# Optimization experiments

Hardware: AMD Instinct MI355X
Metric: run time of the kernel (lower is better)

## Reference

```python
import jax, jax.numpy as jnp
import numpy as np

# Adaptive embedding (Transformer-XL / wt103 config)
N_TOKEN = 267735
D_PROJ = 1024
CUTOFF_ENDS = [0, 20000, 40000, 200000, N_TOKEN]
DIV_VAL = 4
D_EMBS = [1024 // DIV_VAL**i for i in range(4)]  # [1024, 256, 64, 16]
EMB_SCALE = float(D_PROJ) ** 0.5


def setup_inputs() -> dict:
    key = jax.random.key(0)
    ks = jax.random.split(key, 9)
    inp = jax.random.randint(ks[0], (4, 4096), 0, N_TOKEN, dtype=jnp.int64)
    out = {"inp": inp}
    # init_scale=1.0 -> embed std = d_emb_i**-0.5, proj std = d_proj**-0.5
    for i in range(4):
        l, r = CUTOFF_ENDS[i], CUTOFF_ENDS[i + 1]
        d_i = D_EMBS[i]
        out[f"emb{i}"] = (jax.random.normal(ks[1 + i], (r - l, d_i), dtype=jnp.float32)
                           * (d_i ** -0.5))
        out[f"proj{i}"] = (jax.random.normal(ks[5 + i], (D_PROJ, d_i), dtype=jnp.float32)
                            * (D_PROJ ** -0.5))
    return out


def reference(inp, emb0, emb1, emb2, emb3, proj0, proj1, proj2, proj3):
    embs = [emb0, emb1, emb2, emb3]
    projs = [proj0, proj1, proj2, proj3]
    B, S = inp.shape
    out = jnp.zeros((B, S, D_PROJ), dtype=emb0.dtype)
    for i in range(4):
        l, r = CUTOFF_ENDS[i], CUTOFF_ENDS[i + 1]
        mask = (inp >= l) & (inp < r)                      # [B,S]
        idx = jnp.clip(inp - l, 0, r - l - 1)              # in-range local ids
        e = embs[i][idx]                                   # [B,S,d_i]
        p = jnp.einsum('bsd,pd->bsp', e, projs[i])         # [B,S,d_proj]
        out = out + jnp.where(mask[..., None], p, jnp.zeros((), dtype=p.dtype))
    return out * jnp.asarray(EMB_SCALE, dtype=out.dtype)
```

## Files before the change

### kernel.cpp

```cpp
#include <hip/hip_runtime.h>
#include <stdint.h>

#define NTOKENS 16384
#define DPROJ   1024

#define CAP0 2048
#define CAP1 2048
#define CAP2 12288
#define CAP3 6144
#define TOTCAP 22528

typedef __attribute__((ext_vector_type(8))) short bf16x8;
typedef __attribute__((ext_vector_type(4))) float f32x4;

__device__ __forceinline__ unsigned short f2bf(float f) {
    union { float f; uint32_t u; } x; x.f = f;
    uint32_t r = x.u + 0x7FFFu + ((x.u >> 16) & 1u);
    return (unsigned short)(r >> 16);
}

__device__ __forceinline__ int cap_base(int c) {
    return c == 0 ? 0 : c == 1 ? CAP0 : c == 2 ? CAP0 + CAP1 : CAP0 + CAP1 + CAP2;
}
__device__ __forceinline__ int d_orig(int c) { return 1024 >> (2 * c); }
__device__ __forceinline__ int d_pad(int c)  { return c >= 2 ? 64 : (1024 >> (2 * c)); }


__global__ __launch_bounds__(64) void zero_counts(int* counts) {
    if (threadIdx.x < 4) counts[threadIdx.x] = 0;
}

__global__ __launch_bounds__(256) void scatter_tokens(const int* __restrict__ inp,
                                                      int* counts, uint32_t* tokmap) {
    __shared__ int lcnt[4];
    __shared__ int lbase[4];
    const int t = blockIdx.x * 256 + threadIdx.x;
    if (threadIdx.x < 4) lcnt[threadIdx.x] = 0;
    __syncthreads();
    const int v = inp[t];
    int c, lo;
    if (v < 20000)       { c = 0; lo = 0; }
    else if (v < 40000)  { c = 1; lo = 20000; }
    else if (v < 200000) { c = 2; lo = 40000; }
    else                 { c = 3; lo = 200000; }
    const int lr = atomicAdd(&lcnt[c], 1);
    __syncthreads();
    if (threadIdx.x < 4) lbase[threadIdx.x] = atomicAdd(&counts[threadIdx.x], lcnt[threadIdx.x]);
    __syncthreads();
    const int slot = lbase[c] + lr;
    const int cap = (c == 0 || c == 1) ? CAP0 : (c == 2 ? CAP2 : CAP3);
    if (slot < cap)
        tokmap[cap_base(c) + slot] = ((uint32_t)(v - lo) << 14) | (uint32_t)t;
}

__global__ __launch_bounds__(256) void mfma_gemm(
    const float* __restrict__ e0, const float* __restrict__ e1,
    const float* __restrict__ e2, const float* __restrict__ e3,
    const float* __restrict__ p0, const float* __restrict__ p1,
    const float* __restrict__ p2, const float* __restrict__ p3,
    const int* __restrict__ counts, const uint32_t* __restrict__ tokmap,
    float* __restrict__ out)
{
    const int slot = blockIdx.x;
    const int c  = slot < 32 ? 0 : slot < 64 ? 1 : slot < 256 ? 2 : 3;
    const int tm = slot - (c == 0 ? 0 : c == 1 ? 32 : c == 2 ? 64 : 256);
    const int n  = counts[c];
    if (tm * 64 >= n) return;
    const int tn = blockIdx.y;
    const int d  = d_orig(c);
    const int dp = d_pad(c);
    const float* __restrict__ emb  = c == 0 ? e0 : c == 1 ? e1 : c == 2 ? e2 : e3;
    const float* __restrict__ proj = c == 0 ? p0 : c == 1 ? p1 : c == 2 ? p2 : p3;
    const int cb = cap_base(c);

    __shared__ unsigned short Als[64 * 64];
    __shared__ unsigned short Bls[64 * 64];
    __shared__ int aLoc[64];
    __shared__ int aTok[64];

    const int t = threadIdx.x;
    const int w = t >> 6;
    const int l = t & 63;
    const int wr = w >> 1, wc = w & 1;
    const int g   = l >> 4;
    const int sub = l & 15;

    if (t < 64) {
        const int gr = tm * 64 + t;
        if (gr < n) {
            const uint32_t info = tokmap[cb + gr];
            aLoc[t] = (int)(info >> 14);
            aTok[t] = (int)(info & 16383u);
        } else { aLoc[t] = -1; aTok[t] = -1; }
    }
    __syncthreads();

    f32x4 acc[2][2];
    #pragma unroll
    for (int i = 0; i < 2; ++i)
        #pragma unroll
        for (int j = 0; j < 2; ++j) acc[i][j] = (f32x4)0.f;

    for (int k0 = 0; k0 < dp; k0 += 64) {
        const int kk = k0 + sub * 4;
        #pragma unroll
        for (int pass = 0; pass < 4; ++pass) {
            const int row = w * 16 + pass * 4 + g;
            const int loc = aLoc[row];
            float4 v = make_float4(0.f, 0.f, 0.f, 0.f);
            if (loc >= 0 && kk < d)
                v = *reinterpret_cast<const float4*>(emb + (size_t)loc * d + kk);
            ushort4 o; o.x = f2bf(v.x); o.y = f2bf(v.y); o.z = f2bf(v.z); o.w = f2bf(v.w);
            *reinterpret_cast<ushort4*>((char*)Als + row * 128 +
                ((((sub >> 1) ^ (row & 7)) << 4) | ((sub & 1) << 3))) = o;
        }
        #pragma unroll
        for (int pass = 0; pass < 4; ++pass) {
            const int row = w * 16 + pass * 4 + g;
            float4 v = make_float4(0.f, 0.f, 0.f, 0.f);
            if (kk < d)
                v = *reinterpret_cast<const float4*>(proj + (size_t)(tn * 64 + row) * d + kk);
            ushort4 o; o.x = f2bf(v.x); o.y = f2bf(v.y); o.z = f2bf(v.z); o.w = f2bf(v.w);
            *reinterpret_cast<ushort4*>((char*)Bls + row * 128 +
                ((((sub >> 1) ^ (row & 7)) << 4) | ((sub & 1) << 3))) = o;
        }
        __syncthreads();

        bf16x8 af[2][2], bf[2][2];
        #pragma unroll
        for (int fm = 0; fm < 2; ++fm) {
            const int row = wr * 32 + fm * 16 + (l & 15);
            #pragma unroll
            for (int h = 0; h < 2; ++h) {
                const int chunk = h * 4 + (l >> 4);
                af[fm][h] = *reinterpret_cast<const bf16x8*>(
                    (const char*)Als + row * 128 + ((chunk ^ (row & 7)) << 4));
            }
        }
        #pragma unroll
        for (int fn = 0; fn < 2; ++fn) {
            const int row = wc * 32 + fn * 16 + (l & 15);
            #pragma unroll
            for (int h = 0; h < 2; ++h) {
                const int chunk = h * 4 + (l >> 4);
                bf[fn][h] = *reinterpret_cast<const bf16x8*>(
                    (const char*)Bls + row * 128 + ((chunk ^ (row & 7)) << 4));
            }
        }
        #pragma unroll
        for (int fm = 0; fm < 2; ++fm)
            #pragma unroll
            for (int fn = 0; fn < 2; ++fn)
                #pragma unroll
                for (int h = 0; h < 2; ++h)
                    acc[fm][fn] = __builtin_amdgcn_mfma_f32_16x16x32_bf16(
                        af[fm][h], bf[fn][h], acc[fm][fn], 0, 0, 0);
        __syncthreads();
    }

    const float scale = 32.0f;
    #pragma unroll
    for (int fm = 0; fm < 2; ++fm) {
        const int rbase = wr * 32 + fm * 16 + (l >> 4) * 4;
        #pragma unroll
        for (int r = 0; r < 4; ++r) {
            const int row = rbase + r;
            const int tok = aTok[row];
            if (tok >= 0) {
                float* __restrict__ orow =
                    out + (size_t)tok * DPROJ + tn * 64 + wc * 32 + (l & 15);
                #pragma unroll
                for (int fn = 0; fn < 2; ++fn)
                    orow[fn * 16] = acc[fm][fn][r] * scale;
            }
        }
    }
}

extern "C" void kernel_launch(void* const* d_in, const int* in_sizes, int n_in,
                              void* d_out, int out_size, void* d_ws, size_t ws_size,
                              hipStream_t stream) {
    const int* inp = (const int*)d_in[0];
    const float* emb[4];
    const float* proj[4];
    if (in_sizes[2] == 1024 * 1024) {
        for (int i = 0; i < 4; ++i) { emb[i] = (const float*)d_in[1 + 2 * i];
                                      proj[i] = (const float*)d_in[2 + 2 * i]; }
    } else {
        for (int i = 0; i < 4; ++i) { emb[i] = (const float*)d_in[1 + i];
                                      proj[i] = (const float*)d_in[5 + i]; }
    }
    float* out = (float*)d_out;

    int*      counts = (int*)d_ws;
    uint32_t* tokmap = (uint32_t*)((char*)d_ws + 256);

    zero_counts<<<1, 64, 0, stream>>>(counts);
    scatter_tokens<<<NTOKENS / 256, 256, 0, stream>>>(inp, counts, tokmap);
    mfma_gemm<<<dim3(352, 16), 256, 0, stream>>>(
        emb[0], emb[1], emb[2], emb[3],
        proj[0], proj[1], proj[2], proj[3],
        counts, tokmap, out);
}
```

Baseline: 242.6 us.

## Pre-convert projections to bf16, double-buffer LDS, and widen N tile to 128

Adds a kernel that converts all projection matrices to padded bf16 in workspace once per call. The GEMM then stages B tiles directly into LDS with global_load_lds and double-buffers both A and B across K steps, so the next tile's loads overlap with the MFMAs on the current one. The N tile doubles to 128, which halves the number of gathers of the embedding rows. The cost is one extra launch, extra workspace traffic and more LDS and registers per block.

```diff
diff --git a/kernel.cpp b/kernel.cpp
--- a/kernel.cpp
+++ b/kernel.cpp
@@ -19,12 +19,23 @@
     return (unsigned short)(r >> 16);
 }
 
+__device__ __forceinline__ void gl_lds16(const void* g, void* lds) {
+    __builtin_amdgcn_global_load_lds(
+        (const __attribute__((address_space(1))) void*)g,
+        (__attribute__((address_space(3))) void*)lds, 16, 0, 0);
+}
+
 __device__ __forceinline__ int cap_base(int c) {
     return c == 0 ? 0 : c == 1 ? CAP0 : c == 2 ? CAP0 + CAP1 : CAP0 + CAP1 + CAP2;
 }
 __device__ __forceinline__ int d_orig(int c) { return 1024 >> (2 * c); }
 __device__ __forceinline__ int d_pad(int c)  { return c >= 2 ? 64 : (1024 >> (2 * c)); }
-
+__device__ __forceinline__ size_t p_base(int c) {
+    return c == 0 ? 0u : c == 1 ? 1048576u : c == 2 ? 1310720u : 1376256u;
+}
+
+#define WS_TOKMAP 256
+#define WS_PROJ   92160
 
 __global__ __launch_bounds__(64) void zero_counts(int* counts) {
     if (threadIdx.x < 4) counts[threadIdx.x] = 0;
@@ -53,11 +64,29 @@
         tokmap[cap_base(c) + slot] = ((uint32_t)(v - lo) << 14) | (uint32_t)t;
 }
 
+__global__ __launch_bounds__(256) void conv_proj(const float* __restrict__ p0, const float* __restrict__ p1,
+                                                 const float* __restrict__ p2, const float* __restrict__ p3,
+                                                 unsigned short* __restrict__ projws) {
+    const int c = blockIdx.y;
+    const float* __restrict__ src = c == 0 ? p0 : c == 1 ? p1 : c == 2 ? p2 : p3;
+    const int d  = d_orig(c);
+    const int dp = d_pad(c);
+    const int sh = c == 0 ? 10 : c == 1 ? 8 : 6;
+    const int idx4 = (blockIdx.x * 256 + threadIdx.x) * 4;
+    if (idx4 >= 1024 * dp) return;
+    const int row = idx4 >> sh;
+    const int k   = idx4 & (dp - 1);
+    float4 v = make_float4(0.f, 0.f, 0.f, 0.f);
+    if (k < d) v = *reinterpret_cast<const float4*>(src + (size_t)row * d + k);
+    ushort4 o;
+    o.x = f2bf(v.x); o.y = f2bf(v.y); o.z = f2bf(v.z); o.w = f2bf(v.w);
+    *reinterpret_cast<ushort4*>(projws + p_base(c) + idx4) = o;
+}
+
 __global__ __launch_bounds__(256) void mfma_gemm(
     const float* __restrict__ e0, const float* __restrict__ e1,
     const float* __restrict__ e2, const float* __restrict__ e3,
-    const float* __restrict__ p0, const float* __restrict__ p1,
-    const float* __restrict__ p2, const float* __restrict__ p3,
+    const unsigned short* __restrict__ projws,
     const int* __restrict__ counts, const uint32_t* __restrict__ tokmap,
     float* __restrict__ out)
 {
@@ -69,12 +98,13 @@
     const int tn = blockIdx.y;
     const int d  = d_orig(c);
     const int dp = d_pad(c);
-    const float* __restrict__ emb  = c == 0 ? e0 : c == 1 ? e1 : c == 2 ? e2 : e3;
-    const float* __restrict__ proj = c == 0 ? p0 : c == 1 ? p1 : c == 2 ? p2 : p3;
+    const int nsteps = dp >> 6;
+    const float* __restrict__ emb = c == 0 ? e0 : c == 1 ? e1 : c == 2 ? e2 : e3;
+    const unsigned short* __restrict__ Bsrc = projws + p_base(c) + (size_t)(tn * 128) * dp;
     const int cb = cap_base(c);
 
-    __shared__ unsigned short Als[64 * 64];
-    __shared__ unsigned short Bls[64 * 64];
+    __shared__ unsigned short Als[2][64 * 64];
+    __shared__ unsigned short Bls[2][128 * 64];
     __shared__ int aLoc[64];
     __shared__ int aTok[64];
 
@@ -82,8 +112,6 @@
     const int w = t >> 6;
     const int l = t & 63;
     const int wr = w >> 1, wc = w & 1;
-    const int g   = l >> 4;
-    const int sub = l & 15;
 
     if (t < 64) {
         const int gr = tm * 64 + t;
@@ -95,67 +123,102 @@
     }
     __syncthreads();
 
-    f32x4 acc[2][2];
+    const int arow = t >> 2;
+    const int asl0 = t & 3;
+
+    const int bR0   = l >> 3;
+    const int bphys = l & 7;
+    #define STAGE_B(buf, k0)                                                        \
+        do {                                                                        \
+            _Pragma("unroll")                                                       \
+            for (int i_ = 0; i_ < 4; ++i_) {                                        \
+                const int seg_ = w * 4 + i_;                                        \
+                const int R_   = seg_ * 8 + bR0;                                    \
+                const int src_ = bphys ^ (R_ & 7);                                  \
+                gl_lds16(Bsrc + (size_t)R_ * dp + (k0) + src_ * 8,                  \
+                         &Bls[buf][seg_ * 512]);                                    \
+            }                                                                       \
+        } while (0)
+
+    #define LOAD_A(k0, va)                                                          \
+        do {                                                                        \
+            const int loc_ = aLoc[arow];                                            \
+            _Pragma("unroll")                                                       \
+            for (int i_ = 0; i_ < 4; ++i_) {                                        \
+                const int s_  = asl0 + 4 * i_;                                      \
+                const int kk_ = (k0) + s_ * 4;                                      \
+                va[i_] = make_float4(0.f, 0.f, 0.f, 0.f);                           \
+                if (loc_ >= 0 && kk_ < d)                                           \
+                    va[i_] = *reinterpret_cast<const float4*>(                      \
+                        emb + (size_t)loc_ * d + kk_);                              \
+            }                                                                       \
+        } while (0)
+
+    #define WRITE_A(buf, va)                                                        \
+        do {                                                                        \
+            _Pragma("unroll")                                                       \
+            for (int i_ = 0; i_ < 4; ++i_) {                                        \
+                const int s_ = asl0 + 4 * i_;                                       \
+                const int ch_ = (s_ >> 1) ^ (arow & 7);                             \
+                ushort4 o_;                                                         \
+                o_.x = f2bf(va[i_].x); o_.y = f2bf(va[i_].y);                       \
+                o_.z = f2bf(va[i_].z); o_.w = f2bf(va[i_].w);                       \
+                *reinterpret_cast<ushort4*>((char*)&Als[buf][0] + arow * 128 +      \
+                    ch_ * 16 + (s_ & 1) * 8) = o_;                                  \
+            }                                                                       \
+        } while (0)
+
+    f32x4 acc[2][4];
     #pragma unroll
     for (int i = 0; i < 2; ++i)
         #pragma unroll
-        for (int j = 0; j < 2; ++j) acc[i][j] = (f32x4)0.f;
-
-    for (int k0 = 0; k0 < dp; k0 += 64) {
-        const int kk = k0 + sub * 4;
-        #pragma unroll
-        for (int pass = 0; pass < 4; ++pass) {
-            const int row = w * 16 + pass * 4 + g;
-            const int loc = aLoc[row];
-            float4 v = make_float4(0.f, 0.f, 0.f, 0.f);
-            if (loc >= 0 && kk < d)
-                v = *reinterpret_cast<const float4*>(emb + (size_t)loc * d + kk);
-            ushort4 o; o.x = f2bf(v.x); o.y = f2bf(v.y); o.z = f2bf(v.z); o.w = f2bf(v.w);
-            *reinterpret_cast<ushort4*>((char*)Als + row * 128 +
-                ((((sub >> 1) ^ (row & 7)) << 4) | ((sub & 1) << 3))) = o;
-        }
-        #pragma unroll
-        for (int pass = 0; pass < 4; ++pass) {
-            const int row = w * 16 + pass * 4 + g;
-            float4 v = make_float4(0.f, 0.f, 0.f, 0.f);
-            if (kk < d)
-                v = *reinterpret_cast<const float4*>(proj + (size_t)(tn * 64 + row) * d + kk);
-            ushort4 o; o.x = f2bf(v.x); o.y = f2bf(v.y); o.z = f2bf(v.z); o.w = f2bf(v.w);
-            *reinterpret_cast<ushort4*>((char*)Bls + row * 128 +
-                ((((sub >> 1) ^ (row & 7)) << 4) | ((sub & 1) << 3))) = o;
-        }
-        __syncthreads();
-
-        bf16x8 af[2][2], bf[2][2];
+        for (int j = 0; j < 4; ++j) acc[i][j] = (f32x4)0.f;
+
+    float4 va[4];
+    STAGE_B(0, 0);
+    LOAD_A(0, va);
+    WRITE_A(0, va);
+    __syncthreads();
+
+    int cur = 0;
+    for (int k = 0; k < nsteps; ++k) {
+        const int k0n = (k + 1) << 6;
+        if (k + 1 < nsteps) {
+            STAGE_B(cur ^ 1, k0n);
+            LOAD_A(k0n, va);
+        }
+        bf16x8 af[2][2], bf[4][2];
         #pragma unroll
         for (int fm = 0; fm < 2; ++fm) {
             const int row = wr * 32 + fm * 16 + (l & 15);
             #pragma unroll
             for (int h = 0; h < 2; ++h) {
-                const int chunk = h * 4 + (l >> 4);
+                const int chunk = (h * 4 + (l >> 4)) ^ (row & 7);
                 af[fm][h] = *reinterpret_cast<const bf16x8*>(
-                    (const char*)Als + row * 128 + ((chunk ^ (row & 7)) << 4));
+                    (const char*)&Als[cur][0] + row * 128 + chunk * 16);
             }
         }
         #pragma unroll
-        for (int fn = 0; fn < 2; ++fn) {
-            const int row = wc * 32 + fn * 16 + (l & 15);
+        for (int fn = 0; fn < 4; ++fn) {
+            const int row = wc * 64 + fn * 16 + (l & 15);
             #pragma unroll
             for (int h = 0; h < 2; ++h) {
-                const int chunk = h * 4 + (l >> 4);
+                const int chunk = (h * 4 + (l >> 4)) ^ (row & 7);
                 bf[fn][h] = *reinterpret_cast<const bf16x8*>(
-                    (const char*)Bls + row * 128 + ((chunk ^ (row & 7)) << 4));
+                    (const char*)&Bls[cur][0] + row * 128 + chunk * 16);
             }
         }
         #pragma unroll
         for (int fm = 0; fm < 2; ++fm)
             #pragma unroll
-            for (int fn = 0; fn < 2; ++fn)
+            for (int fn = 0; fn < 4; ++fn)
                 #pragma unroll
                 for (int h = 0; h < 2; ++h)
                     acc[fm][fn] = __builtin_amdgcn_mfma_f32_16x16x32_bf16(
                         af[fm][h], bf[fn][h], acc[fm][fn], 0, 0, 0);
+        if (k + 1 < nsteps) WRITE_A(cur ^ 1, va);
         __syncthreads();
+        cur ^= 1;
     }
 
     const float scale = 32.0f;
@@ -164,13 +227,12 @@
         const int rbase = wr * 32 + fm * 16 + (l >> 4) * 4;
         #pragma unroll
         for (int r = 0; r < 4; ++r) {
-            const int row = rbase + r;
-            const int tok = aTok[row];
+            const int tok = aTok[rbase + r];
             if (tok >= 0) {
                 float* __restrict__ orow =
-                    out + (size_t)tok * DPROJ + tn * 64 + wc * 32 + (l & 15);
+                    out + (size_t)tok * DPROJ + tn * 128 + wc * 64 + (l & 15);
                 #pragma unroll
-                for (int fn = 0; fn < 2; ++fn)
+                for (int fn = 0; fn < 4; ++fn)
                     orow[fn * 16] = acc[fm][fn][r] * scale;
             }
         }
@@ -192,13 +254,14 @@
     }
     float* out = (float*)d_out;
 
-    int*      counts = (int*)d_ws;
-    uint32_t* tokmap = (uint32_t*)((char*)d_ws + 256);
+    int*            counts = (int*)d_ws;
+    uint32_t*       tokmap = (uint32_t*)((char*)d_ws + WS_TOKMAP);
+    unsigned short* projws = (unsigned short*)((char*)d_ws + WS_PROJ);
 
     zero_counts<<<1, 64, 0, stream>>>(counts);
     scatter_tokens<<<NTOKENS / 256, 256, 0, stream>>>(inp, counts, tokmap);
-    mfma_gemm<<<dim3(352, 16), 256, 0, stream>>>(
+    conv_proj<<<dim3(1024, 4), 256, 0, stream>>>(proj[0], proj[1], proj[2], proj[3], projws);
+    mfma_gemm<<<dim3(352, 8), 256, 0, stream>>>(
         emb[0], emb[1], emb[2], emb[3],
-        proj[0], proj[1], proj[2], proj[3],
-        counts, tokmap, out);
-}
+        projws, counts, tokmap, out);
+}
```

Measured after the change: 208.2 us. -14.2%, faster.

## Pre-convert projections to bf16 and load MFMA operands directly from global

Applied to the files above, without the earlier changes.

Adds a pre-pass that converts all projection matrices to bf16 in workspace, folded into the counts-zeroing launch. The GEMM now drops LDS staging and barriers: each lane loads its A fragment straight from the gathered embedding rows, converting to bf16 in registers, and loads B fragments directly from the bf16 projection buffer. The N tile is doubled to 128, so the grid has half as many columns, and the kernel gets a launch-bounds occupancy hint. The aim is to cut repeated fp32 projection reads and conversions plus LDS sync overhead. The cost is uncoalesced per-lane global loads with no reuse through shared memory, and an extra conversion pass over about 1.4M elements on every call.

```diff
diff --git a/kernel.cpp b/kernel.cpp
--- a/kernel.cpp
+++ b/kernel.cpp
@@ -22,12 +22,31 @@
 __device__ __forceinline__ int cap_base(int c) {
     return c == 0 ? 0 : c == 1 ? CAP0 : c == 2 ? CAP0 + CAP1 : CAP0 + CAP1 + CAP2;
 }
-__device__ __forceinline__ int d_orig(int c) { return 1024 >> (2 * c); }
-__device__ __forceinline__ int d_pad(int c)  { return c >= 2 ? 64 : (1024 >> (2 * c)); }
+#define PB1 1048576
+#define PB2 1310720
+#define PB3 1376256
+#define PEND 1392640
+__device__ __forceinline__ size_t p_base(int c) {
+    return c == 0 ? 0u : c == 1 ? (size_t)PB1 : c == 2 ? (size_t)PB2 : (size_t)PB3;
+}
 
+#define WS_TOKMAP 256
+#define WS_PROJ   92160
 
-__global__ __launch_bounds__(64) void zero_counts(int* counts) {
-    if (threadIdx.x < 4) counts[threadIdx.x] = 0;
+__global__ __launch_bounds__(256) void conv_zero(
+    const float* __restrict__ p0, const float* __restrict__ p1,
+    const float* __restrict__ p2, const float* __restrict__ p3,
+    int* counts, unsigned short* __restrict__ projws)
+{
+    if (blockIdx.x == 0 && threadIdx.x < 4) counts[threadIdx.x] = 0;
+    const int idx4 = (blockIdx.x * 256 + threadIdx.x) * 4;
+    const int c = idx4 < PB1 ? 0 : idx4 < PB2 ? 1 : idx4 < PB3 ? 2 : 3;
+    const float* __restrict__ src = c == 0 ? p0 : c == 1 ? p1 : c == 2 ? p2 : p3;
+    const int local = idx4 - (int)p_base(c);
+    float4 v = *reinterpret_cast<const float4*>(src + local);
+    ushort4 o;
+    o.x = f2bf(v.x); o.y = f2bf(v.y); o.z = f2bf(v.z); o.w = f2bf(v.w);
+    *reinterpret_cast<ushort4*>(projws + idx4) = o;
 }
 
 __global__ __launch_bounds__(256) void scatter_tokens(const int* __restrict__ inp,
@@ -53,11 +72,10 @@
         tokmap[cap_base(c) + slot] = ((uint32_t)(v - lo) << 14) | (uint32_t)t;
 }
 
-__global__ __launch_bounds__(256) void mfma_gemm(
+__global__ __launch_bounds__(256, 4) void mfma_gemm(
     const float* __restrict__ e0, const float* __restrict__ e1,
     const float* __restrict__ e2, const float* __restrict__ e3,
-    const float* __restrict__ p0, const float* __restrict__ p1,
-    const float* __restrict__ p2, const float* __restrict__ p3,
+    const unsigned short* __restrict__ projws,
     const int* __restrict__ counts, const uint32_t* __restrict__ tokmap,
     float* __restrict__ out)
 {
@@ -67,110 +85,86 @@
     const int n  = counts[c];
     if (tm * 64 >= n) return;
     const int tn = blockIdx.y;
-    const int d  = d_orig(c);
-    const int dp = d_pad(c);
-    const float* __restrict__ emb  = c == 0 ? e0 : c == 1 ? e1 : c == 2 ? e2 : e3;
-    const float* __restrict__ proj = c == 0 ? p0 : c == 1 ? p1 : c == 2 ? p2 : p3;
+    const int d  = 1024 >> (2 * c);
+    const float* __restrict__ emb = c == 0 ? e0 : c == 1 ? e1 : c == 2 ? e2 : e3;
+    const unsigned short* __restrict__ Bsrc = projws + p_base(c) + (size_t)(tn * 128) * d;
     const int cb = cap_base(c);
-
-    __shared__ unsigned short Als[64 * 64];
-    __shared__ unsigned short Bls[64 * 64];
-    __shared__ int aLoc[64];
-    __shared__ int aTok[64];
 
     const int t = threadIdx.x;
     const int w = t >> 6;
     const int l = t & 63;
     const int wr = w >> 1, wc = w & 1;
-    const int g   = l >> 4;
-    const int sub = l & 15;
+    const int lr = l & 15;
+    const int lg = l >> 4;
 
-    if (t < 64) {
-        const int gr = tm * 64 + t;
-        if (gr < n) {
-            const uint32_t info = tokmap[cb + gr];
-            aLoc[t] = (int)(info >> 14);
-            aTok[t] = (int)(info & 16383u);
-        } else { aLoc[t] = -1; aTok[t] = -1; }
+    const float* arow0;
+    const float* arow1;
+    {
+        const int g0 = tm * 64 + wr * 32 + lr;
+        const int g1 = g0 + 16;
+        arow0 = (g0 < n) ? emb + (size_t)(tokmap[cb + g0] >> 14) * d : nullptr;
+        arow1 = (g1 < n) ? emb + (size_t)(tokmap[cb + g1] >> 14) * d : nullptr;
     }
-    __syncthreads();
 
-    f32x4 acc[2][2];
+    f32x4 acc[2][4];
     #pragma unroll
     for (int i = 0; i < 2; ++i)
         #pragma unroll
-        for (int j = 0; j < 2; ++j) acc[i][j] = (f32x4)0.f;
+        for (int j = 0; j < 4; ++j) acc[i][j] = (f32x4)0.f;
 
-    for (int k0 = 0; k0 < dp; k0 += 64) {
-        const int kk = k0 + sub * 4;
+    const int nsteps = (d + 63) >> 6;
+    for (int s = 0; s < nsteps; ++s) {
         #pragma unroll
-        for (int pass = 0; pass < 4; ++pass) {
-            const int row = w * 16 + pass * 4 + g;
-            const int loc = aLoc[row];
-            float4 v = make_float4(0.f, 0.f, 0.f, 0.f);
-            if (loc >= 0 && kk < d)
-                v = *reinterpret_cast<const float4*>(emb + (size_t)loc * d + kk);
-            ushort4 o; o.x = f2bf(v.x); o.y = f2bf(v.y); o.z = f2bf(v.z); o.w = f2bf(v.w);
-            *reinterpret_cast<ushort4*>((char*)Als + row * 128 +
-                ((((sub >> 1) ^ (row & 7)) << 4) | ((sub & 1) << 3))) = o;
-        }
-        #pragma unroll
-        for (int pass = 0; pass < 4; ++pass) {
-            const int row = w * 16 + pass * 4 + g;
-            float4 v = make_float4(0.f, 0.f, 0.f, 0.f);
-            if (kk < d)
-                v = *reinterpret_cast<const float4*>(proj + (size_t)(tn * 64 + row) * d + kk);
-            ushort4 o; o.x = f2bf(v.x); o.y = f2bf(v.y); o.z = f2bf(v.z); o.w = f2bf(v.w);
-            *reinterpret_cast<ushort4*>((char*)Bls + row * 128 +
-                ((((sub >> 1) ^ (row & 7)) << 4) | ((sub & 1) << 3))) = o;
-        }
-        __syncthreads();
-
-        bf16x8 af[2][2], bf[2][2];
-        #pragma unroll
-        for (int fm = 0; fm < 2; ++fm) {
-            const int row = wr * 32 + fm * 16 + (l & 15);
-            #pragma unroll
-            for (int h = 0; h < 2; ++h) {
-                const int chunk = h * 4 + (l >> 4);
-                af[fm][h] = *reinterpret_cast<const bf16x8*>(
-                    (const char*)Als + row * 128 + ((chunk ^ (row & 7)) << 4));
+        for (int h = 0; h < 2; ++h) {
+            if (s * 64 + h * 32 < d) {
+                const int kA = s * 64 + h * 32 + lg * 8;
+                const bool kv = kA < d;
+                bf16x8 af[2], bf[4];
+                #pragma unroll
+                for (int fm = 0; fm < 2; ++fm) {
+                    const float* ap = fm ? arow1 : arow0;
+                    float4 u0 = make_float4(0.f, 0.f, 0.f, 0.f);
+                    float4 u1 = u0;
+                    if (kv && ap) {
+                        u0 = *reinterpret_cast<const float4*>(ap + kA);
+                        u1 = *reinterpret_cast<const float4*>(ap + kA + 4);
+                    }
+                    bf16x8 r;
+                    r[0] = (short)f2bf(u0.x); r[1] = (short)f2bf(u0.y);
+                    r[2] = (short)f2bf(u0.z); r[3] = (short)f2bf(u0.w);
+                    r[4] = (short)f2bf(u1.x); r[5] = (short)f2bf(u1.y);
+                    r[6] = (short)f2bf(u1.z); r[7] = (short)f2bf(u1.w);
+                    af[fm] = r;
+                }
+                #pragma unroll
+                for (int fn = 0; fn < 4; ++fn) {
+                    const int br = wc * 64 + fn * 16 + lr;
+                    bf[fn] = kv ? *reinterpret_cast<const bf16x8*>(Bsrc + (size_t)br * d + kA)
+                                : (bf16x8)(short)0;
+                }
+                #pragma unroll
+                for (int fm = 0; fm < 2; ++fm)
+                    #pragma unroll
+                    for (int fn = 0; fn < 4; ++fn)
+                        acc[fm][fn] = __builtin_amdgcn_mfma_f32_16x16x32_bf16(
+                            af[fm], bf[fn], acc[fm][fn], 0, 0, 0);
             }
         }
-        #pragma unroll
-        for (int fn = 0; fn < 2; ++fn) {
-            const int row = wc * 32 + fn * 16 + (l & 15);
-            #pragma unroll
-            for (int h = 0; h < 2; ++h) {
-                const int chunk = h * 4 + (l >> 4);
-                bf[fn][h] = *reinterpret_cast<const bf16x8*>(
-                    (const char*)Bls + row * 128 + ((chunk ^ (row & 7)) << 4));
-            }
-        }
-        #pragma unroll
-        for (int fm = 0; fm < 2; ++fm)
-            #pragma unroll
-            for (int fn = 0; fn < 2; ++fn)
-                #pragma unroll
-                for (int h = 0; h < 2; ++h)
-                    acc[fm][fn] = __builtin_amdgcn_mfma_f32_16x16x32_bf16(
-                        af[fm][h], bf[fn][h], acc[fm][fn], 0, 0, 0);
-        __syncthreads();
     }
 
     const float scale = 32.0f;
     #pragma unroll
     for (int fm = 0; fm < 2; ++fm) {
-        const int rbase = wr * 32 + fm * 16 + (l >> 4) * 4;
+        const int rbase = tm * 64 + wr * 32 + fm * 16 + lg * 4;
         #pragma unroll
         for (int r = 0; r < 4; ++r) {
-            const int row = rbase + r;
-            const int tok = aTok[row];
-            if (tok >= 0) {
+            const int gr = rbase + r;
+            if (gr < n) {
+                const int tok = (int)(tokmap[cb + gr] & 16383u);
                 float* __restrict__ orow =
-                    out + (size_t)tok * DPROJ + tn * 64 + wc * 32 + (l & 15);
+                    out + (size_t)tok * DPROJ + tn * 128 + wc * 64 + lr;
                 #pragma unroll
-                for (int fn = 0; fn < 2; ++fn)
+                for (int fn = 0; fn < 4; ++fn)
                     orow[fn * 16] = acc[fm][fn][r] * scale;
             }
         }
@@ -192,13 +186,13 @@
     }
     float* out = (float*)d_out;
 
-    int*      counts = (int*)d_ws;
-    uint32_t* tokmap = (uint32_t*)((char*)d_ws + 256);
+    int*            counts = (int*)d_ws;
+    uint32_t*       tokmap = (uint32_t*)((char*)d_ws + WS_TOKMAP);
+    unsigned short* projws = (unsigned short*)((char*)d_ws + WS_PROJ);
 
-    zero_counts<<<1, 64, 0, stream>>>(counts);
+    conv_zero<<<1360, 256, 0, stream>>>(proj[0], proj[1], proj[2], proj[3], counts, projws);
     scatter_tokens<<<NTOKENS / 256, 256, 0, stream>>>(inp, counts, tokmap);
-    mfma_gemm<<<dim3(352, 16), 256, 0, stream>>>(
+    mfma_gemm<<<dim3(352, 8), 256, 0, stream>>>(
         emb[0], emb[1], emb[2], emb[3],
-        proj[0], proj[1], proj[2], proj[3],
-        counts, tokmap, out);
+        projws, counts, tokmap, out);
 }
```

After: 266.6 us. +9.9%, slower.
